# Performance work log

Hardware: AMD Instinct MI355X
Metric: run time of the kernel (lower is better)

## Reference

```python
import jax, jax.numpy as jnp
import numpy as np

N = 100_000   # nodes
E = 1_600_000 # edges
IN, H, OUT = 128, 128, 128
G = 64        # graphs in batch
EPS = 1e-5    # batchnorm eps


def setup_inputs() -> dict:
    key = jax.random.key(0)
    ks = jax.random.split(key, 16)
    x = jax.random.normal(ks[0], (N, IN), dtype=jnp.float32)
    edge_index = jax.random.randint(ks[1], (2, E), 0, N, dtype=jnp.int32)
    batch = jnp.sort(jax.random.randint(ks[2], (N,), 0, G, dtype=jnp.int32))
    def lin(k, fi, fo):
        return jax.random.normal(k, (fi, fo), dtype=jnp.float32) / np.sqrt(fi).astype(np.float32)
    inp = {
        'x': x, 'edge_index': edge_index, 'batch': batch,
        'W1': lin(ks[3], IN, H), 'b1': jnp.zeros((H,), jnp.float32),
        'g1': jnp.ones((H,), jnp.float32), 'beta1': jnp.zeros((H,), jnp.float32),
        'W2': lin(ks[4], H, H), 'b2': jnp.zeros((H,), jnp.float32),
        'g2': jnp.ones((H,), jnp.float32), 'beta2': jnp.zeros((H,), jnp.float32),
        'W3': lin(ks[5], H, H), 'b3': jnp.zeros((H,), jnp.float32),
        'g3': jnp.ones((H,), jnp.float32), 'beta3': jnp.zeros((H,), jnp.float32),
        'fc_w': lin(ks[6], H, OUT), 'fc_b': jnp.zeros((OUT,), jnp.float32),
    }
    return inp


def _gcn_prep(edge_index):
    # add self loops, compute symmetric normalization (shared across layers)
    loop = jnp.arange(N, dtype=edge_index.dtype)
    row = jnp.concatenate([edge_index[0], loop])  # source
    col = jnp.concatenate([edge_index[1], loop])  # target
    deg = jax.ops.segment_sum(jnp.ones_like(col, dtype=jnp.float32), col, num_segments=N)
    dinv = jnp.where(deg > 0, jax.lax.rsqrt(deg), 0.0)
    norm = dinv[row] * dinv[col]  # (E+N,)
    return row, col, norm


def _gcn_bn_relu(h, W, b, g, beta, row, col, norm):
    hw = h @ W                                           # (N, H)
    msg = norm[:, None] * hw[row]                        # gather + scale
    h = jax.ops.segment_sum(msg, col, num_segments=N) + b  # scatter-add
    # BatchNorm1d (training-mode batch statistics, biased var)
    mu = jnp.mean(h, axis=0)
    var = jnp.mean(jnp.square(h - mu), axis=0)
    h = g * (h - mu) * jax.lax.rsqrt(var + EPS) + beta
    return jax.nn.relu(h)


def reference(x, edge_index, batch, W1, b1, g1, beta1, W2, b2, g2, beta2,
              W3, b3, g3, beta3, fc_w, fc_b):
    row, col, norm = _gcn_prep(edge_index)
    h = _gcn_bn_relu(x, W1, b1, g1, beta1, row, col, norm)
    h = _gcn_bn_relu(h, W2, b2, g2, beta2, row, col, norm)
    h = _gcn_bn_relu(h, W3, b3, g3, beta3, row, col, norm)
    # global_mean_pool over batch assignment
    sums = jax.ops.segment_sum(h, batch, num_segments=G)
    cnt = jax.ops.segment_sum(jnp.ones((N,), jnp.float32), batch, num_segments=G)
    pooled = sums / jnp.maximum(cnt, 1.0)[:, None]       # (G, H)
    return pooled @ fc_w + fc_b                          # (G, OUT)
```

## Files before the change

### kernel.cpp

```cpp
#include <hip/hip_runtime.h>

#define NN 100000
#define EE 1600000
#define HH 128
#define GG 64
#define TOT (EE + NN)
#define PSPLIT 8
#define NB 782
#define BCAP 4096
#define FCHUNK 4096

typedef __attribute__((ext_vector_type(8))) short s16x8;
typedef __attribute__((ext_vector_type(4))) float f32x4;

__device__ __forceinline__ unsigned short f2bf(float f) {
    unsigned u = __float_as_uint(f);
    u = u + 0x7FFFu + ((u >> 16) & 1u);
    return (unsigned short)(u >> 16);
}


__global__ void init_kernel(int* bucketCnt, int* gstart, int* gend, float* poolsum) {
    int i = blockIdx.x * blockDim.x + threadIdx.x;
    if (i < NB) bucketCnt[i] = 0;
    if (i < GG) { gstart[i] = NN; gend[i] = 0; }
    if (i < GG * HH) poolsum[i] = 0.f;
}

__global__ __launch_bounds__(256) void hist_kernel(const int* __restrict__ ei, int* bucketCnt) {
    __shared__ int h[NB];
    int tid = threadIdx.x;
    for (int i = tid; i < NB; i += 256) h[i] = 0;
    __syncthreads();
    for (int e = blockIdx.x * 256 + tid; e < EE; e += gridDim.x * 256) {
        unsigned c = (unsigned)ei[EE + e];
        if (c < NN) atomicAdd(&h[c >> 7], 1);
    }
    __syncthreads();
    for (int i = tid; i < NB; i += 256) {
        int v = h[i];
        if (v) atomicAdd(&bucketCnt[i], v);
    }
}

__global__ void bscan_kernel(const int* __restrict__ bucketCnt, int* __restrict__ bucketEdgeStart,
                             int* __restrict__ bucketSlotStart, int* __restrict__ cursor,
                             int* __restrict__ col_start) {
    __shared__ int se[1024], ss[1024];
    int t = threadIdx.x;
    int ec = (t < NB) ? bucketCnt[t] : 0;
    int nc = (t < NB) ? min(128, NN - t * 128) : 0;
    se[t] = ec; ss[t] = ec + nc;
    __syncthreads();
    for (int off = 1; off < 1024; off <<= 1) {
        int a = 0, b = 0;
        if (t >= off) { a = se[t - off]; b = ss[t - off]; }
        __syncthreads();
        se[t] += a; ss[t] += b;
        __syncthreads();
    }
    if (t < NB) {
        bucketEdgeStart[t] = se[t] - ec;
        bucketSlotStart[t] = ss[t] - (ec + nc);
        cursor[t] = se[t] - ec;
    }
    if (t == NB - 1) col_start[NN] = ss[t];
}

__global__ __launch_bounds__(256) void bfill2_kernel(const int* __restrict__ ei, int* cursor,
                                                     unsigned* __restrict__ ebuf) {
    __shared__ int h[NB];
    __shared__ int lbase[NB];
    int tid = threadIdx.x;
    size_t e0 = (size_t)blockIdx.x * FCHUNK;
    for (int i = tid; i < NB; i += 256) h[i] = 0;
    __syncthreads();
    unsigned r[16], c[16];
#pragma unroll
    for (int k = 0; k < 16; ++k) {
        size_t e = e0 + (size_t)k * 256 + tid;
        unsigned rr = 0xFFFFFFFFu, cc = 0;
        if (e < EE) {
            rr = (unsigned)ei[e];
            cc = (unsigned)ei[EE + e];
            if (rr >= NN || cc >= NN) rr = 0xFFFFFFFFu;
        }
        r[k] = rr; c[k] = cc;
        if (rr != 0xFFFFFFFFu) atomicAdd(&h[cc >> 7], 1);
    }
    __syncthreads();
    for (int i = tid; i < NB; i += 256) {
        int cnt = h[i];
        lbase[i] = cnt ? atomicAdd(&cursor[i], cnt) : 0;
    }
    __syncthreads();
    for (int i = tid; i < NB; i += 256) h[i] = 0;
    __syncthreads();
#pragma unroll
    for (int k = 0; k < 16; ++k) {
        if (r[k] != 0xFFFFFFFFu) {
            unsigned cc = c[k];
            int b = cc >> 7;
            int slot = lbase[b] + atomicAdd(&h[b], 1);
            if (slot >= 0 && slot < EE) ebuf[slot] = (r[k] << 7) | (cc & 127u);
        }
    }
}

__global__ __launch_bounds__(256) void bproc_kernel(const unsigned* __restrict__ ebuf,
                                                    const int* __restrict__ bucketCnt,
                                                    const int* __restrict__ bucketEdgeStart,
                                                    const int* __restrict__ bucketSlotStart,
                                                    int* __restrict__ col_start,
                                                    float* __restrict__ dinv,
                                                    int* __restrict__ srcv) {
    __shared__ unsigned s_e[BCAP];
    __shared__ int s_cnt[128], s_scan[128], s_cur[128];
    int b = blockIdx.x;
    int tid = threadIdx.x;
    int n0 = b * 128;
    int nb = min(128, NN - n0);
    int est = bucketEdgeStart[b];
    int ecnt = min(bucketCnt[b], BCAP);
    if (tid < 128) s_cnt[tid] = 0;
    __syncthreads();
    for (int i = tid; i < ecnt; i += 256) {
        unsigned v = ebuf[est + i];
        s_e[i] = v;
        atomicAdd(&s_cnt[v & 127u], 1);
    }
    __syncthreads();
    int myc = 0;
    if (tid < 128) {
        myc = (tid < nb) ? s_cnt[tid] + 1 : 0;
        s_scan[tid] = myc;
    }
    __syncthreads();
    for (int off = 1; off < 128; off <<= 1) {
        int a = 0;
        if (tid < 128 && tid >= off) a = s_scan[tid - off];
        __syncthreads();
        if (tid < 128) s_scan[tid] += a;
        __syncthreads();
    }
    if (tid < nb) {
        int slotbase = bucketSlotStart[b] + s_scan[tid] - myc;
        col_start[n0 + tid] = slotbase;
        dinv[n0 + tid] = rsqrtf((float)(s_cnt[tid] + 1));
        srcv[slotbase] = n0 + tid;
        s_cur[tid] = slotbase + 1;
    }
    __syncthreads();
    for (int i = tid; i < ecnt; i += 256) {
        unsigned v = s_e[i];
        int slot = atomicAdd(&s_cur[v & 127u], 1);
        srcv[slot] = (int)(v >> 7);
    }
}

__global__ void bounds_kernel(const int* __restrict__ batch, int* gstart, int* gend) {
    int i = blockIdx.x * blockDim.x + threadIdx.x;
    if (i >= NN) return;
    int b = batch[i];
    if (i == 0) {
        gstart[b] = 0;
    } else {
        int bp = batch[i - 1];
        if (b != bp) {
            gstart[b] = i;
            gend[bp] = i;
        }
    }
    if (i == NN - 1) gend[b] = NN;
}

__global__ void wprep_kernel(const float* __restrict__ W0, const float* __restrict__ W1,
                             const float* __restrict__ W2, unsigned short* __restrict__ Wt) {
    int i = blockIdx.x * 256 + threadIdx.x;
    int l = i >> 14;
    int r = i & 16383;
    if (l < 3) {
        const float* W = (l == 0) ? W0 : (l == 1) ? W1 : W2;
        int k = r >> 7, n = r & 127;
        Wt[l * HH * HH + n * HH + k] = f2bf(W[r]);
    }
}

__global__ void cast_kernel(const float* __restrict__ x, unsigned* __restrict__ Xbf) {
    int i = blockIdx.x * blockDim.x + threadIdx.x;
    if (i >= NN * 64) return;
    float2 v = ((const float2*)x)[i];
    Xbf[i] = (unsigned)f2bf(v.x) | ((unsigned)f2bf(v.y) << 16);
}


__global__ __launch_bounds__(256) void agg_kernel(const uint4* __restrict__ Xbf4,
                                                  const int* __restrict__ col_start,
                                                  const int* __restrict__ srcv,
                                                  const float* __restrict__ dinv,
                                                  unsigned short* __restrict__ Abf,
                                                  float* __restrict__ gsum,
                                                  float* __restrict__ gsq) {
    if (blockIdx.x == 0 && threadIdx.x < HH) {
        gsum[threadIdx.x] = 0.f;
        gsq[threadIdx.x] = 0.f;
    }
    int wid = (int)((blockIdx.x * blockDim.x + threadIdx.x) >> 6);
    int lane = threadIdx.x & 63;
    if (wid >= NN) return;
    int s0 = col_start[wid], s1 = col_start[wid + 1];
    float dd = dinv[wid];
    int q = lane >> 4;
    int l16 = lane & 15;
    float acc[8];
#pragma unroll
    for (int j = 0; j < 8; ++j) acc[j] = 0.f;

    for (int base = s0; base < s1; base += 64) {
        int cnt = min(64, s1 - base);
        int msrc = 0;
        float mw = 0.f;
        if (lane < cnt) { msrc = srcv[base + lane]; mw = dinv[msrc] * dd; }
        int rounds = (cnt + 3) >> 2;
        int p = 0;
        for (; p + 4 <= rounds; p += 4) {
            uint4 u[4];
            float w[4];
#pragma unroll
            for (int k = 0; k < 4; ++k) {
                int idx = (p + k) * 4 + q;
                int src = __shfl(msrc, idx);
                w[k] = __shfl(mw, idx);
                u[k] = Xbf4[(size_t)src * 16 + l16];
            }
#pragma unroll
            for (int k = 0; k < 4; ++k) {
                acc[0] += w[k] * __uint_as_float(u[k].x << 16);
                acc[1] += w[k] * __uint_as_float(u[k].x & 0xFFFF0000u);
                acc[2] += w[k] * __uint_as_float(u[k].y << 16);
                acc[3] += w[k] * __uint_as_float(u[k].y & 0xFFFF0000u);
                acc[4] += w[k] * __uint_as_float(u[k].z << 16);
                acc[5] += w[k] * __uint_as_float(u[k].z & 0xFFFF0000u);
                acc[6] += w[k] * __uint_as_float(u[k].w << 16);
                acc[7] += w[k] * __uint_as_float(u[k].w & 0xFFFF0000u);
            }
        }
        for (; p < rounds; ++p) {
            int idx = p * 4 + q;
            int src = __shfl(msrc, idx);
            float w = __shfl(mw, idx);
            uint4 u = Xbf4[(size_t)src * 16 + l16];
            acc[0] += w * __uint_as_float(u.x << 16);
            acc[1] += w * __uint_as_float(u.x & 0xFFFF0000u);
            acc[2] += w * __uint_as_float(u.y << 16);
            acc[3] += w * __uint_as_float(u.y & 0xFFFF0000u);
            acc[4] += w * __uint_as_float(u.z << 16);
            acc[5] += w * __uint_as_float(u.z & 0xFFFF0000u);
            acc[6] += w * __uint_as_float(u.w << 16);
            acc[7] += w * __uint_as_float(u.w & 0xFFFF0000u);
        }
    }
#pragma unroll
    for (int j = 0; j < 8; ++j) {
        acc[j] += __shfl_xor(acc[j], 16);
        acc[j] += __shfl_xor(acc[j], 32);
    }
    if (q == 0) {
        uint4 pk;
        pk.x = (unsigned)f2bf(acc[0]) | ((unsigned)f2bf(acc[1]) << 16);
        pk.y = (unsigned)f2bf(acc[2]) | ((unsigned)f2bf(acc[3]) << 16);
        pk.z = (unsigned)f2bf(acc[4]) | ((unsigned)f2bf(acc[5]) << 16);
        pk.w = (unsigned)f2bf(acc[6]) | ((unsigned)f2bf(acc[7]) << 16);
        ((uint4*)Abf)[(size_t)wid * 16 + l16] = pk;
    }
}

__global__ __launch_bounds__(256) void gemm_stats_kernel(const unsigned short* __restrict__ Abf,
                                                         const unsigned short* __restrict__ Wt,
                                                         const float* __restrict__ bias,
                                                         float* __restrict__ gsum,
                                                         float* __restrict__ gsq) {
    __shared__ unsigned short wlds[128 * 136];
    __shared__ float ssum[HH], ssq[HH];
    int tid = threadIdx.x;
    if (tid < HH) { ssum[tid] = 0.f; ssq[tid] = 0.f; }
#pragma unroll
    for (int it = 0; it < 16; ++it) {
        int idx = it * 256 + tid;
        int r = idx >> 5, c = idx & 31;
        *(uint2*)&wlds[r * 136 + c * 4] = *(const uint2*)(Wt + r * HH + c * 4);
    }
    __syncthreads();

    int lane = tid & 63;
    int wave = tid >> 6;
    int mcol = lane & 15;
    int quad = lane >> 4;
    int rowbase = blockIdx.x * 128 + wave * 32;
    int row0 = rowbase + mcol;
    int row1 = row0 + 16;

    f32x4 acc[2][8];
#pragma unroll
    for (int mt = 0; mt < 2; ++mt)
#pragma unroll
        for (int nt = 0; nt < 8; ++nt) acc[mt][nt] = (f32x4){0.f, 0.f, 0.f, 0.f};

    s16x8 zf = {0, 0, 0, 0, 0, 0, 0, 0};
#pragma unroll
    for (int ks = 0; ks < 4; ++ks) {
        int k0 = ks * 32 + quad * 8;
        s16x8 a0 = (row0 < NN) ? *(const s16x8*)(Abf + (size_t)row0 * HH + k0) : zf;
        s16x8 a1 = (row1 < NN) ? *(const s16x8*)(Abf + (size_t)row1 * HH + k0) : zf;
#pragma unroll
        for (int nt = 0; nt < 8; ++nt) {
            s16x8 b = *(const s16x8*)&wlds[(nt * 16 + mcol) * 136 + k0];
            acc[0][nt] = __builtin_amdgcn_mfma_f32_16x16x32_bf16(a0, b, acc[0][nt], 0, 0, 0);
            acc[1][nt] = __builtin_amdgcn_mfma_f32_16x16x32_bf16(a1, b, acc[1][nt], 0, 0, 0);
        }
    }

    float s[8], sq[8];
#pragma unroll
    for (int nt = 0; nt < 8; ++nt) { s[nt] = 0.f; sq[nt] = 0.f; }
#pragma unroll
    for (int mt = 0; mt < 2; ++mt) {
        int rbase = rowbase + mt * 16 + quad * 4;
#pragma unroll
        for (int nt = 0; nt < 8; ++nt) {
            float bv = bias[nt * 16 + mcol];
            f32x4 a = acc[mt][nt];
#pragma unroll
            for (int reg = 0; reg < 4; ++reg) {
                if (rbase + reg < NN) {
                    float h = a[reg] + bv;
                    s[nt] += h; sq[nt] += h * h;
                }
            }
        }
    }
#pragma unroll
    for (int nt = 0; nt < 8; ++nt) {
        float v = s[nt];  v += __shfl_xor(v, 16);  v += __shfl_xor(v, 32);
        float w = sq[nt]; w += __shfl_xor(w, 16);  w += __shfl_xor(w, 32);
        if (quad == 0) {
            atomicAdd(&ssum[nt * 16 + mcol], v);
            atomicAdd(&ssq[nt * 16 + mcol], w);
        }
    }
    __syncthreads();
    if (tid < HH) {
        atomicAdd(&gsum[tid], ssum[tid]);
        atomicAdd(&gsq[tid], ssq[tid]);
    }
}

__global__ __launch_bounds__(256) void gemm_apply_kernel(const unsigned short* __restrict__ Abf,
                                                         const unsigned short* __restrict__ Wt,
                                                         const float* __restrict__ bias,
                                                         const float* __restrict__ gsum,
                                                         const float* __restrict__ gsq,
                                                         const float* __restrict__ g,
                                                         const float* __restrict__ beta,
                                                         unsigned short* __restrict__ Xb16) {
    __shared__ unsigned short wlds[128 * 136];
    __shared__ float asc[HH], bsh[HH];
    int tid = threadIdx.x;
#pragma unroll
    for (int it = 0; it < 16; ++it) {
        int idx = it * 256 + tid;
        int r = idx >> 5, c = idx & 31;
        *(uint2*)&wlds[r * 136 + c * 4] = *(const uint2*)(Wt + r * HH + c * 4);
    }
    if (tid < HH) {
        float mu = gsum[tid] * (1.f / (float)NN);
        float var = fmaxf(gsq[tid] * (1.f / (float)NN) - mu * mu, 0.f);
        float a = g[tid] * rsqrtf(var + 1e-5f);
        asc[tid] = a;
        bsh[tid] = a * (bias[tid] - mu) + beta[tid];
    }
    __syncthreads();

    int lane = tid & 63;
    int wave = tid >> 6;
    int mcol = lane & 15;
    int quad = lane >> 4;
    int rowbase = blockIdx.x * 128 + wave * 32;
    int row0 = rowbase + mcol;
    int row1 = row0 + 16;

    f32x4 acc[2][8];
#pragma unroll
    for (int mt = 0; mt < 2; ++mt)
#pragma unroll
        for (int nt = 0; nt < 8; ++nt) acc[mt][nt] = (f32x4){0.f, 0.f, 0.f, 0.f};

    s16x8 zf = {0, 0, 0, 0, 0, 0, 0, 0};
#pragma unroll
    for (int ks = 0; ks < 4; ++ks) {
        int k0 = ks * 32 + quad * 8;
        s16x8 a0 = (row0 < NN) ? *(const s16x8*)(Abf + (size_t)row0 * HH + k0) : zf;
        s16x8 a1 = (row1 < NN) ? *(const s16x8*)(Abf + (size_t)row1 * HH + k0) : zf;
#pragma unroll
        for (int nt = 0; nt < 8; ++nt) {
            s16x8 b = *(const s16x8*)&wlds[(nt * 16 + mcol) * 136 + k0];
            acc[0][nt] = __builtin_amdgcn_mfma_f32_16x16x32_bf16(a0, b, acc[0][nt], 0, 0, 0);
            acc[1][nt] = __builtin_amdgcn_mfma_f32_16x16x32_bf16(a1, b, acc[1][nt], 0, 0, 0);
        }
    }

#pragma unroll
    for (int mt = 0; mt < 2; ++mt) {
        int rbase = rowbase + mt * 16 + quad * 4;
#pragma unroll
        for (int nt = 0; nt < 8; ++nt) {
            int col = nt * 16 + mcol;
            float av = asc[col], bv = bsh[col];
            f32x4 a = acc[mt][nt];
#pragma unroll
            for (int reg = 0; reg < 4; ++reg) {
                int r = rbase + reg;
                if (r < NN) {
                    float o = fmaxf(av * a[reg] + bv, 0.f);
                    Xb16[(size_t)r * HH + col] = f2bf(o);
                }
            }
        }
    }
}


__global__ void pool_kernel(const unsigned* __restrict__ Xbf, const int* __restrict__ gstart,
                            const int* __restrict__ gend, float* __restrict__ poolsum) {
    int g = blockIdx.x;
    int sp = blockIdx.y;
    int t = threadIdx.x;
    int s = gstart[g], e = gend[g];
    if (e <= s) return;
    int len = e - s;
    int chunk = (len + PSPLIT - 1) / PSPLIT;
    int cs = s + sp * chunk;
    int ce = min(cs + chunk, e);
    if (cs >= ce) return;
    float2 acc = make_float2(0.f, 0.f);
    for (int i = cs; i < ce; ++i) {
        unsigned u = Xbf[(size_t)i * 64 + t];
        acc.x += __uint_as_float(u << 16);
        acc.y += __uint_as_float(u & 0xFFFF0000u);
    }
    atomicAdd(&poolsum[g * HH + 2 * t], acc.x);
    atomicAdd(&poolsum[g * HH + 2 * t + 1], acc.y);
}

__global__ void fc_kernel(const float* __restrict__ poolsum, const int* __restrict__ gstart,
                          const int* __restrict__ gend, const float* __restrict__ fc_w,
                          const float* __restrict__ fc_b, float* __restrict__ out) {
    int g = blockIdx.x;
    int o = threadIdx.x;
    int cnt = gend[g] - gstart[g];
    float inv = (cnt > 0) ? (1.f / (float)cnt) : 0.f;
    float acc = fc_b[o];
    for (int k = 0; k < HH; ++k) acc += (poolsum[g * HH + k] * inv) * fc_w[k * HH + o];
    out[g * HH + o] = acc;
}


extern "C" void kernel_launch(void* const* d_in, const int* in_sizes, int n_in,
                              void* d_out, int out_size, void* d_ws, size_t ws_size,
                              hipStream_t stream) {
    const float* x     = (const float*)d_in[0];
    const int*   ei    = (const int*)d_in[1];
    const int*   batch = (const int*)d_in[2];
    const float* Wl[3]    = {(const float*)d_in[3], (const float*)d_in[7], (const float*)d_in[11]};
    const float* bl[3]    = {(const float*)d_in[4], (const float*)d_in[8], (const float*)d_in[12]};
    const float* gl[3]    = {(const float*)d_in[5], (const float*)d_in[9], (const float*)d_in[13]};
    const float* betal[3] = {(const float*)d_in[6], (const float*)d_in[10], (const float*)d_in[14]};
    const float* fc_w = (const float*)d_in[15];
    const float* fc_b = (const float*)d_in[16];
    float* out = (float*)d_out;

    char* ws = (char*)d_ws;
    size_t off = 0;
    auto take = [&](size_t n) -> void* {
        void* p = ws + off;
        off = (off + n + 255) & ~(size_t)255;
        return p;
    };
    int*   bucketCnt       = (int*)take((size_t)NB * 4);
    int*   bucketEdgeStart = (int*)take((size_t)NB * 4);
    int*   bucketSlotStart = (int*)take((size_t)NB * 4);
    int*   cursor          = (int*)take((size_t)NB * 4);
    unsigned* ebuf         = (unsigned*)take((size_t)EE * 4);
    int*   col_start       = (int*)take((size_t)(NN + 1) * 4);
    float* dinv            = (float*)take((size_t)NN * 4);
    int*   srcv            = (int*)take((size_t)TOT * 4);
    float* gsum            = (float*)take(HH * 4);
    float* gsq             = (float*)take(HH * 4);
    int*   gstart          = (int*)take(GG * 4);
    int*   gend            = (int*)take(GG * 4);
    float* poolsum         = (float*)take((size_t)GG * HH * 4);
    unsigned short* wt     = (unsigned short*)take((size_t)3 * HH * HH * 2);
    unsigned* Xbf          = (unsigned*)take((size_t)NN * 64 * 4);
    unsigned short* Abf    = (unsigned short*)take((size_t)NN * HH * 2);

    init_kernel<<<(NN + 255) / 256, 256, 0, stream>>>(bucketCnt, gstart, gend, poolsum);
    hist_kernel<<<512, 256, 0, stream>>>(ei, bucketCnt);
    bscan_kernel<<<1, 1024, 0, stream>>>(bucketCnt, bucketEdgeStart, bucketSlotStart, cursor, col_start);
    bfill2_kernel<<<(EE + FCHUNK - 1) / FCHUNK, 256, 0, stream>>>(ei, cursor, ebuf);
    bproc_kernel<<<NB, 256, 0, stream>>>(ebuf, bucketCnt, bucketEdgeStart, bucketSlotStart,
                                         col_start, dinv, srcv);
    bounds_kernel<<<(NN + 255) / 256, 256, 0, stream>>>(batch, gstart, gend);
    wprep_kernel<<<(3 * HH * HH + 255) / 256, 256, 0, stream>>>(Wl[0], Wl[1], Wl[2], wt);
    cast_kernel<<<(NN * 64 + 255) / 256, 256, 0, stream>>>(x, Xbf);

    for (int l = 0; l < 3; ++l) {
        const unsigned short* W = wt + (size_t)l * HH * HH;
        agg_kernel<<<(NN * 64 + 255) / 256, 256, 0, stream>>>((const uint4*)Xbf, col_start, srcv,
                                                              dinv, Abf, gsum, gsq);
        gemm_stats_kernel<<<(NN + 127) / 128, 256, 0, stream>>>(Abf, W, bl[l], gsum, gsq);
        gemm_apply_kernel<<<(NN + 127) / 128, 256, 0, stream>>>(Abf, W, bl[l], gsum, gsq,
                                                                gl[l], betal[l],
                                                                (unsigned short*)Xbf);
    }

    pool_kernel<<<dim3(GG, PSPLIT), 64, 0, stream>>>(Xbf, gstart, gend, poolsum);
    fc_kernel<<<GG, 128, 0, stream>>>(poolsum, gstart, gend, fc_w, fc_b, out);
}
```

Measured before the change: 571.7 us.

## Drop edge histogram pass, merge setup kernels, store pre-BN activations for elementwise apply

Edge bucketing now uses fixed-capacity slots per bucket (BCAP), so the separate histogram pass over edge targets goes away. Bucket counts are recovered from the cursors afterwards, and the scan moves after the fill. The x cast, weight transpose, pool zeroing and graph-bound computation (now a binary search on the sorted batch) are merged into one setup kernel, cutting several launches. The GEMM+stats kernel now writes the pre-BN output as bf16 in place, and a light elementwise apply kernel replaces the second full GEMM pass. The cost is an extra bf16 rounding of the pre-normalisation values and scattered 2-byte stores in the GEMM epilogue.

Result: slower. 585.5 us (+2.4%).

```diff
diff --git a/kernel.cpp b/kernel.cpp
--- a/kernel.cpp
+++ b/kernel.cpp
@@ -20,51 +20,38 @@
 }
 
 
-__global__ void init_kernel(int* bucketCnt, int* gstart, int* gend, float* poolsum) {
-    int i = blockIdx.x * blockDim.x + threadIdx.x;
-    if (i < NB) bucketCnt[i] = 0;
-    if (i < GG) { gstart[i] = NN; gend[i] = 0; }
+__global__ __launch_bounds__(256) void setup_kernel(const float* __restrict__ x,
+                                                    const int* __restrict__ batch,
+                                                    const float* __restrict__ W0,
+                                                    const float* __restrict__ W1,
+                                                    const float* __restrict__ W2,
+                                                    unsigned* __restrict__ Xbf,
+                                                    int* __restrict__ cursor,
+                                                    int* __restrict__ gstart, int* __restrict__ gend,
+                                                    float* __restrict__ poolsum,
+                                                    unsigned short* __restrict__ Wt) {
+    int i = blockIdx.x * 256 + threadIdx.x;
+    if (i < NN * 64) {
+        float2 v = ((const float2*)x)[i];
+        Xbf[i] = (unsigned)f2bf(v.x) | ((unsigned)f2bf(v.y) << 16);
+    }
+    if (i < NB) cursor[i] = i * BCAP;
     if (i < GG * HH) poolsum[i] = 0.f;
-}
-
-__global__ __launch_bounds__(256) void hist_kernel(const int* __restrict__ ei, int* bucketCnt) {
-    __shared__ int h[NB];
-    int tid = threadIdx.x;
-    for (int i = tid; i < NB; i += 256) h[i] = 0;
-    __syncthreads();
-    for (int e = blockIdx.x * 256 + tid; e < EE; e += gridDim.x * 256) {
-        unsigned c = (unsigned)ei[EE + e];
-        if (c < NN) atomicAdd(&h[c >> 7], 1);
-    }
-    __syncthreads();
-    for (int i = tid; i < NB; i += 256) {
-        int v = h[i];
-        if (v) atomicAdd(&bucketCnt[i], v);
-    }
-}
-
-__global__ void bscan_kernel(const int* __restrict__ bucketCnt, int* __restrict__ bucketEdgeStart,
-                             int* __restrict__ bucketSlotStart, int* __restrict__ cursor,
-                             int* __restrict__ col_start) {
-    __shared__ int se[1024], ss[1024];
-    int t = threadIdx.x;
-    int ec = (t < NB) ? bucketCnt[t] : 0;
-    int nc = (t < NB) ? min(128, NN - t * 128) : 0;
-    se[t] = ec; ss[t] = ec + nc;
-    __syncthreads();
-    for (int off = 1; off < 1024; off <<= 1) {
-        int a = 0, b = 0;
-        if (t >= off) { a = se[t - off]; b = ss[t - off]; }
-        __syncthreads();
-        se[t] += a; ss[t] += b;
-        __syncthreads();
-    }
-    if (t < NB) {
-        bucketEdgeStart[t] = se[t] - ec;
-        bucketSlotStart[t] = ss[t] - (ec + nc);
-        cursor[t] = se[t] - ec;
-    }
-    if (t == NB - 1) col_start[NN] = ss[t];
+    if (i < GG) {
+        int lo = 0, hi = NN;
+        while (lo < hi) { int m = (lo + hi) >> 1; if (batch[m] < i) lo = m + 1; else hi = m; }
+        int s = lo;
+        lo = 0; hi = NN;
+        while (lo < hi) { int m = (lo + hi) >> 1; if (batch[m] < i + 1) lo = m + 1; else hi = m; }
+        gstart[i] = s;
+        gend[i] = lo;
+    }
+    if (i < 3 * HH * HH) {
+        int l = i >> 14, r = i & 16383;
+        const float* W = (l == 0) ? W0 : (l == 1) ? W1 : W2;
+        int k = r >> 7, n = r & 127;
+        Wt[l * HH * HH + n * HH + k] = f2bf(W[r]);
+    }
 }
 
 __global__ __launch_bounds__(256) void bfill2_kernel(const int* __restrict__ ei, int* cursor,
@@ -102,14 +89,36 @@
             unsigned cc = c[k];
             int b = cc >> 7;
             int slot = lbase[b] + atomicAdd(&h[b], 1);
-            if (slot >= 0 && slot < EE) ebuf[slot] = (r[k] << 7) | (cc & 127u);
-        }
-    }
+            if (slot >= b * BCAP && slot < (b + 1) * BCAP)
+                ebuf[slot] = (r[k] << 7) | (cc & 127u);
+        }
+    }
+}
+
+__global__ void bscan_kernel(const int* __restrict__ cursor, int* __restrict__ bucketSlotStart,
+                             int* __restrict__ col_start) {
+    __shared__ int ss[1024];
+    int t = threadIdx.x;
+    int ec = 0, nc = 0;
+    if (t < NB) {
+        ec = min(max(cursor[t] - t * BCAP, 0), BCAP);
+        nc = min(128, NN - t * 128);
+    }
+    ss[t] = ec + nc;
+    __syncthreads();
+    for (int off = 1; off < 1024; off <<= 1) {
+        int a = 0;
+        if (t >= off) a = ss[t - off];
+        __syncthreads();
+        ss[t] += a;
+        __syncthreads();
+    }
+    if (t < NB) bucketSlotStart[t] = ss[t] - (ec + nc);
+    if (t == NB - 1) col_start[NN] = ss[t];
 }
 
 __global__ __launch_bounds__(256) void bproc_kernel(const unsigned* __restrict__ ebuf,
-                                                    const int* __restrict__ bucketCnt,
-                                                    const int* __restrict__ bucketEdgeStart,
+                                                    const int* __restrict__ cursor,
                                                     const int* __restrict__ bucketSlotStart,
                                                     int* __restrict__ col_start,
                                                     float* __restrict__ dinv,
@@ -120,8 +129,8 @@
     int tid = threadIdx.x;
     int n0 = b * 128;
     int nb = min(128, NN - n0);
-    int est = bucketEdgeStart[b];
-    int ecnt = min(bucketCnt[b], BCAP);
+    int est = b * BCAP;
+    int ecnt = min(max(cursor[b] - est, 0), BCAP);
     if (tid < 128) s_cnt[tid] = 0;
     __syncthreads();
     for (int i = tid; i < ecnt; i += 256) {
@@ -156,41 +165,6 @@
         int slot = atomicAdd(&s_cur[v & 127u], 1);
         srcv[slot] = (int)(v >> 7);
     }
-}
-
-__global__ void bounds_kernel(const int* __restrict__ batch, int* gstart, int* gend) {
-    int i = blockIdx.x * blockDim.x + threadIdx.x;
-    if (i >= NN) return;
-    int b = batch[i];
-    if (i == 0) {
-        gstart[b] = 0;
-    } else {
-        int bp = batch[i - 1];
-        if (b != bp) {
-            gstart[b] = i;
-            gend[bp] = i;
-        }
-    }
-    if (i == NN - 1) gend[b] = NN;
-}
-
-__global__ void wprep_kernel(const float* __restrict__ W0, const float* __restrict__ W1,
-                             const float* __restrict__ W2, unsigned short* __restrict__ Wt) {
-    int i = blockIdx.x * 256 + threadIdx.x;
-    int l = i >> 14;
-    int r = i & 16383;
-    if (l < 3) {
-        const float* W = (l == 0) ? W0 : (l == 1) ? W1 : W2;
-        int k = r >> 7, n = r & 127;
-        Wt[l * HH * HH + n * HH + k] = f2bf(W[r]);
-    }
-}
-
-__global__ void cast_kernel(const float* __restrict__ x, unsigned* __restrict__ Xbf) {
-    int i = blockIdx.x * blockDim.x + threadIdx.x;
-    if (i >= NN * 64) return;
-    float2 v = ((const float2*)x)[i];
-    Xbf[i] = (unsigned)f2bf(v.x) | ((unsigned)f2bf(v.y) << 16);
 }
 
 
@@ -275,7 +249,7 @@
     }
 }
 
-__global__ __launch_bounds__(256) void gemm_stats_kernel(const unsigned short* __restrict__ Abf,
+__global__ __launch_bounds__(256) void gemm_stats_kernel(unsigned short* __restrict__ Abf,
                                                          const unsigned short* __restrict__ Wt,
                                                          const float* __restrict__ bias,
                                                          float* __restrict__ gsum,
@@ -328,12 +302,15 @@
         int rbase = rowbase + mt * 16 + quad * 4;
 #pragma unroll
         for (int nt = 0; nt < 8; ++nt) {
-            float bv = bias[nt * 16 + mcol];
+            int col = nt * 16 + mcol;
+            float bv = bias[col];
             f32x4 a = acc[mt][nt];
 #pragma unroll
             for (int reg = 0; reg < 4; ++reg) {
-                if (rbase + reg < NN) {
+                int r = rbase + reg;
+                if (r < NN) {
                     float h = a[reg] + bv;
+                    Abf[(size_t)r * HH + col] = f2bf(h);
                     s[nt] += h; sq[nt] += h * h;
                 }
             }
@@ -355,78 +332,40 @@
     }
 }
 
-__global__ __launch_bounds__(256) void gemm_apply_kernel(const unsigned short* __restrict__ Abf,
-                                                         const unsigned short* __restrict__ Wt,
-                                                         const float* __restrict__ bias,
-                                                         const float* __restrict__ gsum,
-                                                         const float* __restrict__ gsq,
-                                                         const float* __restrict__ g,
-                                                         const float* __restrict__ beta,
-                                                         unsigned short* __restrict__ Xb16) {
-    __shared__ unsigned short wlds[128 * 136];
+__global__ __launch_bounds__(256) void apply_kernel(const unsigned short* __restrict__ Hb,
+                                                    const float* __restrict__ gsum,
+                                                    const float* __restrict__ gsq,
+                                                    const float* __restrict__ g,
+                                                    const float* __restrict__ beta,
+                                                    unsigned short* __restrict__ Xb16) {
     __shared__ float asc[HH], bsh[HH];
     int tid = threadIdx.x;
-#pragma unroll
-    for (int it = 0; it < 16; ++it) {
-        int idx = it * 256 + tid;
-        int r = idx >> 5, c = idx & 31;
-        *(uint2*)&wlds[r * 136 + c * 4] = *(const uint2*)(Wt + r * HH + c * 4);
-    }
     if (tid < HH) {
         float mu = gsum[tid] * (1.f / (float)NN);
         float var = fmaxf(gsq[tid] * (1.f / (float)NN) - mu * mu, 0.f);
         float a = g[tid] * rsqrtf(var + 1e-5f);
         asc[tid] = a;
-        bsh[tid] = a * (bias[tid] - mu) + beta[tid];
-    }
-    __syncthreads();
-
-    int lane = tid & 63;
-    int wave = tid >> 6;
-    int mcol = lane & 15;
-    int quad = lane >> 4;
-    int rowbase = blockIdx.x * 128 + wave * 32;
-    int row0 = rowbase + mcol;
-    int row1 = row0 + 16;
-
-    f32x4 acc[2][8];
-#pragma unroll
-    for (int mt = 0; mt < 2; ++mt)
-#pragma unroll
-        for (int nt = 0; nt < 8; ++nt) acc[mt][nt] = (f32x4){0.f, 0.f, 0.f, 0.f};
-
-    s16x8 zf = {0, 0, 0, 0, 0, 0, 0, 0};
-#pragma unroll
-    for (int ks = 0; ks < 4; ++ks) {
-        int k0 = ks * 32 + quad * 8;
-        s16x8 a0 = (row0 < NN) ? *(const s16x8*)(Abf + (size_t)row0 * HH + k0) : zf;
-        s16x8 a1 = (row1 < NN) ? *(const s16x8*)(Abf + (size_t)row1 * HH + k0) : zf;
-#pragma unroll
-        for (int nt = 0; nt < 8; ++nt) {
-            s16x8 b = *(const s16x8*)&wlds[(nt * 16 + mcol) * 136 + k0];
-            acc[0][nt] = __builtin_amdgcn_mfma_f32_16x16x32_bf16(a0, b, acc[0][nt], 0, 0, 0);
-            acc[1][nt] = __builtin_amdgcn_mfma_f32_16x16x32_bf16(a1, b, acc[1][nt], 0, 0, 0);
-        }
-    }
-
-#pragma unroll
-    for (int mt = 0; mt < 2; ++mt) {
-        int rbase = rowbase + mt * 16 + quad * 4;
-#pragma unroll
-        for (int nt = 0; nt < 8; ++nt) {
-            int col = nt * 16 + mcol;
-            float av = asc[col], bv = bsh[col];
-            f32x4 a = acc[mt][nt];
-#pragma unroll
-            for (int reg = 0; reg < 4; ++reg) {
-                int r = rbase + reg;
-                if (r < NN) {
-                    float o = fmaxf(av * a[reg] + bv, 0.f);
-                    Xb16[(size_t)r * HH + col] = f2bf(o);
-                }
-            }
-        }
-    }
+        bsh[tid] = beta[tid] - a * mu;
+    }
+    __syncthreads();
+    int i = blockIdx.x * 256 + tid;
+    if (i >= NN * 16) return;
+    int c8 = (i & 15) * 8;
+    uint4 u = ((const uint4*)Hb)[i];
+    unsigned w[4] = {u.x, u.y, u.z, u.w};
+    unsigned r[4];
+#pragma unroll
+    for (int k = 0; k < 4; ++k) {
+        int c = c8 + 2 * k;
+        float h0 = __uint_as_float(w[k] << 16);
+        float h1 = __uint_as_float(w[k] & 0xFFFF0000u);
+        float o0 = fmaxf(asc[c] * h0 + bsh[c], 0.f);
+        float o1 = fmaxf(asc[c + 1] * h1 + bsh[c + 1], 0.f);
+        r[k] = (unsigned)f2bf(o0) | ((unsigned)f2bf(o1) << 16);
+    }
+    uint4 o;
+    o.x = r[0]; o.y = r[1]; o.z = r[2]; o.w = r[3];
+    ((uint4*)Xb16)[i] = o;
 }
 
 
@@ -486,11 +425,9 @@
         off = (off + n + 255) & ~(size_t)255;
         return p;
     };
-    int*   bucketCnt       = (int*)take((size_t)NB * 4);
-    int*   bucketEdgeStart = (int*)take((size_t)NB * 4);
     int*   bucketSlotStart = (int*)take((size_t)NB * 4);
     int*   cursor          = (int*)take((size_t)NB * 4);
-    unsigned* ebuf         = (unsigned*)take((size_t)EE * 4);
+    unsigned* ebuf         = (unsigned*)take((size_t)NB * BCAP * 4);
     int*   col_start       = (int*)take((size_t)(NN + 1) * 4);
     float* dinv            = (float*)take((size_t)NN * 4);
     int*   srcv            = (int*)take((size_t)TOT * 4);
@@ -503,22 +440,18 @@
     unsigned* Xbf          = (unsigned*)take((size_t)NN * 64 * 4);
     unsigned short* Abf    = (unsigned short*)take((size_t)NN * HH * 2);
 
-    init_kernel<<<(NN + 255) / 256, 256, 0, stream>>>(bucketCnt, gstart, gend, poolsum);
-    hist_kernel<<<512, 256, 0, stream>>>(ei, bucketCnt);
-    bscan_kernel<<<1, 1024, 0, stream>>>(bucketCnt, bucketEdgeStart, bucketSlotStart, cursor, col_start);
+    setup_kernel<<<(NN * 64 + 255) / 256, 256, 0, stream>>>(x, batch, Wl[0], Wl[1], Wl[2],
+                                                            Xbf, cursor, gstart, gend, poolsum, wt);
     bfill2_kernel<<<(EE + FCHUNK - 1) / FCHUNK, 256, 0, stream>>>(ei, cursor, ebuf);
-    bproc_kernel<<<NB, 256, 0, stream>>>(ebuf, bucketCnt, bucketEdgeStart, bucketSlotStart,
-                                         col_start, dinv, srcv);
-    bounds_kernel<<<(NN + 255) / 256, 256, 0, stream>>>(batch, gstart, gend);
-    wprep_kernel<<<(3 * HH * HH + 255) / 256, 256, 0, stream>>>(Wl[0], Wl[1], Wl[2], wt);
-    cast_kernel<<<(NN * 64 + 255) / 256, 256, 0, stream>>>(x, Xbf);
+    bscan_kernel<<<1, 1024, 0, stream>>>(cursor, bucketSlotStart, col_start);
+    bproc_kernel<<<NB, 256, 0, stream>>>(ebuf, cursor, bucketSlotStart, col_start, dinv, srcv);
 
     for (int l = 0; l < 3; ++l) {
         const unsigned short* W = wt + (size_t)l * HH * HH;
         agg_kernel<<<(NN * 64 + 255) / 256, 256, 0, stream>>>((const uint4*)Xbf, col_start, srcv,
                                                               dinv, Abf, gsum, gsq);
         gemm_stats_kernel<<<(NN + 127) / 128, 256, 0, stream>>>(Abf, W, bl[l], gsum, gsq);
-        gemm_apply_kernel<<<(NN + 127) / 128, 256, 0, stream>>>(Abf, W, bl[l], gsum, gsq,
+        apply_kernel<<<(NN * 16 + 255) / 256, 256, 0, stream>>>(Abf, gsum, gsq,
                                                                 gl[l], betal[l],
                                                                 (unsigned short*)Xbf);
     }
```
